# Optimization experiments

Measured on AMD Instinct MI355X. Metric: run time of the kernel, lower is better.

## Reference

```python
import jax, jax.numpy as jnp
import numpy as np

N_HEAD = 16
HEAD = 64
EMBED = 1024
TOP_K_RATIO = 0.1
MASKED = True
B, T = 2, 2048


def setup_inputs() -> dict:
    key = jax.random.key(0)
    ks = jax.random.split(key, 7)
    w = lambda k, shape: jax.random.normal(k, shape, jnp.float32) * 0.02
    return {
        "index": jax.random.normal(ks[0], (B, T, EMBED), jnp.float32),
        "memory": jax.random.normal(ks[1], (B, T, EMBED), jnp.float32),
        "Wq": w(ks[2], (N_HEAD, EMBED, HEAD)),
        "Wk": w(ks[3], (N_HEAD, EMBED, HEAD)),
        "Wv": w(ks[4], (N_HEAD, EMBED, HEAD)),
        "W_proj": w(ks[5], (N_HEAD * HEAD, EMBED)),
        "b_proj": jnp.zeros((EMBED,), jnp.float32),
    }


def reference(index, memory, Wq, Wk, Wv, W_proj, b_proj):
    b, t, e = index.shape
    s = memory.shape[1]
    # All heads batched: [B, H, T, D]
    q = jnp.einsum("bte,hed->bhtd", index, Wq)
    k = jnp.einsum("bse,hed->bhsd", memory, Wk)
    v = jnp.einsum("bse,hed->bhsd", memory, Wv)
    scores = jnp.einsum("bhtd,bhsd->bhts", q, k) * (HEAD ** -0.5)  # [B,H,T,S]
    neg_inf = jnp.array(-jnp.inf, scores.dtype)
    if MASKED:
        causal = jnp.tril(jnp.ones((t, s), bool))
        scores = jnp.where(causal, scores, neg_inf)
    # top-k sparsification: keep only the top ceil(ratio*S) scores per query row
    k_top = max(1, int(TOP_K_RATIO * s))
    thresh = jax.lax.top_k(scores, k_top)[0][..., -1:]  # kth largest per row
    scores = jnp.where(scores >= thresh, scores, neg_inf)
    att = jax.nn.softmax(scores, axis=-1)
    out = jnp.einsum("bhts,bhsd->bhtd", att, v)
    # concat heads along feature dim: [B, T, H*D]
    out = out.transpose(0, 2, 1, 3).reshape(b, t, N_HEAD * HEAD)
    return out @ W_proj + b_proj  # dropout is identity at eval
```

## Files before the change

kernel.cpp:

```cpp
#include <hip/hip_runtime.h>
#include <hip/hip_bf16.h>

#define TT 2048
#define KTOP 204
#define ROWS 16
#define SCS 2056

typedef float f32x4 __attribute__((ext_vector_type(4)));
typedef short short8 __attribute__((ext_vector_type(8)));
typedef unsigned short u16;
typedef unsigned int u32;
typedef u32 u32x2 __attribute__((ext_vector_type(2)));
typedef u32 u32x4 __attribute__((ext_vector_type(4)));

#define NEG_INF (-__builtin_inff())

static __device__ __forceinline__ f32x4 mfma16(short8 a, short8 b, f32x4 c) {
  return __builtin_amdgcn_mfma_f32_16x16x32_bf16(a, b, c, 0, 0, 0);
}

static __device__ __forceinline__ u16 f2b(float f) {
  __hip_bfloat16 h = __float2bfloat16(f);
  return *reinterpret_cast<u16*>(&h);
}

static __device__ __forceinline__ u32 pack_bf16(float a, float b) {
  u32 ua = __float_as_uint(a), ub = __float_as_uint(b);
  ua = (ua + 0x7FFFu + ((ua >> 16) & 1u)) >> 16;
  ub = (ub + 0x7FFFu + ((ub >> 16) & 1u)) & 0xFFFF0000u;
  return ua | ub;
}

#define GLOAD16(gp, lp) __builtin_amdgcn_global_load_lds( \
    (const __attribute__((address_space(1))) void*)(gp),  \
    (__attribute__((address_space(3))) void*)(lp), 16, 0, 0)

#define WSYNC() do { __builtin_amdgcn_wave_barrier(); \
    asm volatile("s_waitcnt lgkmcnt(0)" ::: "memory"); \
    __builtin_amdgcn_wave_barrier(); } while (0)

static __device__ __forceinline__ void rank64(u32 cnt, int lane, int& k,
                                              u32& dig) {
  int suf = (int)cnt;
#pragma unroll
  for (int off = 1; off < 64; off <<= 1) {
    int o = __shfl_down(suf, off);
    suf += (lane + off < 64) ? o : 0;
  }
  int above = suf - (int)cnt;
  bool found = (above < k) && (above + (int)cnt >= k);
  unsigned long long ball = __ballot(found);
  int src = __ffsll((long long)ball) - 1;
  int nk = k - above;
  k = __shfl(nk, src);
  dig = (u32)src;
}

template <int JMAX>
static __device__ __forceinline__ void select_softmax(
    u16* __restrict__ sc, const u32* __restrict__ hist1,
    u32* __restrict__ hist2, const u32* __restrict__ rowmaxk,
    float* __restrict__ rs, int w, int lane, int t0) {
  const int NI = JMAX * 4;
  int row0 = w, row1 = w + 8;
  int n0 = t0 + row0 + 1, n1 = t0 + row1 + 1;
  bool sel0 = n0 > KTOP, sel1 = n1 > KTOP;

  u32 rv0[NI], rv1[NI];
#pragma unroll
  for (int j = 0; j < JMAX; ++j) {
    u32x4 v0 = *(const u32x4*)&sc[row0 * SCS + lane * 8 + j * 512];
    u32x4 v1 = *(const u32x4*)&sc[row1 * SCS + lane * 8 + j * 512];
    rv0[j*4+0] = v0[0]; rv0[j*4+1] = v0[1]; rv0[j*4+2] = v0[2]; rv0[j*4+3] = v0[3];
    rv1[j*4+0] = v1[0]; rv1[j*4+1] = v1[1]; rv1[j*4+2] = v1[2]; rv1[j*4+3] = v1[3];
  }

  u32 keyth0 = 0, keyth1 = 0;
  int k0 = KTOP, k1 = KTOP;
  u32 pfx0 = 0, pfx1 = 0, d;
  u32 c0 = 0, c1 = 0;
  if (lane < 16) {
    u32x4 q0 = *(const u32x4*)&hist1[lane * 64 + row0 * 4];
    u32x4 q1 = *(const u32x4*)&hist1[lane * 64 + row1 * 4];
    c0 = q0[0] + q0[1] + q0[2] + q0[3];
    c1 = q1[0] + q1[1] + q1[2] + q1[3];
  }
  if (sel0) { rank64(c0, lane, k0, d); pfx0 = d; }
  if (sel1) { rank64(c1, lane, k1, d); pfx1 = d; }

  u32* h2a = &hist2[(w * 2 + 0) * 64];
  u32* h2b = &hist2[(w * 2 + 1) * 64];
  h2a[lane] = 0; h2b[lane] = 0;
  WSYNC();
#pragma unroll
  for (int i = 0; i < NI; ++i) {
    u32 p0 = rv0[i], p1 = rv1[i];
    u32 a0 = p0 & 0xFFFFu, a1 = p0 >> 16;
    u32 b0 = p1 & 0xFFFFu, b1 = p1 >> 16;
    if (sel0) {
      if ((a0 >> 12) == pfx0) atomicAdd(&h2a[(a0 >> 6) & 63u], 1u);
      if ((a1 >> 12) == pfx0) atomicAdd(&h2a[(a1 >> 6) & 63u], 1u);
    }
    if (sel1) {
      if ((b0 >> 12) == pfx1) atomicAdd(&h2b[(b0 >> 6) & 63u], 1u);
      if ((b1 >> 12) == pfx1) atomicAdd(&h2b[(b1 >> 6) & 63u], 1u);
    }
  }
  WSYNC();
  if (sel0) { rank64(h2a[lane], lane, k0, d); pfx0 = (pfx0 << 6) | d; }
  if (sel1) { rank64(h2b[lane], lane, k1, d); pfx1 = (pfx1 << 6) | d; }
  h2a[lane] = 0; h2b[lane] = 0;
  WSYNC();
#pragma unroll
  for (int i = 0; i < NI; ++i) {
    u32 p0 = rv0[i], p1 = rv1[i];
    u32 a0 = p0 & 0xFFFFu, a1 = p0 >> 16;
    u32 b0 = p1 & 0xFFFFu, b1 = p1 >> 16;
    if (sel0) {
      if ((a0 >> 6) == pfx0) atomicAdd(&h2a[a0 & 63u], 1u);
      if ((a1 >> 6) == pfx0) atomicAdd(&h2a[a1 & 63u], 1u);
    }
    if (sel1) {
      if ((b0 >> 6) == pfx1) atomicAdd(&h2b[b0 & 63u], 1u);
      if ((b1 >> 6) == pfx1) atomicAdd(&h2b[b1 & 63u], 1u);
    }
  }
  WSYNC();
  if (sel0) { rank64(h2a[lane], lane, k0, d); keyth0 = (pfx0 << 6) | d; }
  if (sel1) { rank64(h2b[lane], lane, k1, d); keyth1 = (pfx1 << 6) | d; }

  u32 thr0 = keyth0 > 1u ? keyth0 : 1u;
  u32 thr1 = keyth1 > 1u ? keyth1 : 1u;
  u32 kmx0 = rowmaxk[row0], kmx1 = rowmaxk[row1];
  const float c2 = 1.44269504f / 4096.f;
  float sum0 = 0.f, sum1 = 0.f;
#pragma unroll
  for (int i = 0; i < NI; ++i) {
    u32 p0 = rv0[i], p1 = rv1[i];
    u32 a0 = p0 & 0xFFFFu, a1 = p0 >> 16;
    u32 b0 = p1 & 0xFFFFu, b1 = p1 >> 16;
    float pa0 = (a0 >= thr0) ? exp2f((float)(int)(a0 - kmx0) * c2) : 0.f;
    float pa1 = (a1 >= thr0) ? exp2f((float)(int)(a1 - kmx0) * c2) : 0.f;
    float pb0 = (b0 >= thr1) ? exp2f((float)(int)(b0 - kmx1) * c2) : 0.f;
    float pb1 = (b1 >= thr1) ? exp2f((float)(int)(b1 - kmx1) * c2) : 0.f;
    sum0 += pa0 + pa1;
    sum1 += pb0 + pb1;
    rv0[i] = pack_bf16(pa0, pa1);
    rv1[i] = pack_bf16(pb0, pb1);
  }
#pragma unroll
  for (int off = 32; off; off >>= 1) {
    sum0 += __shfl_xor(sum0, off);
    sum1 += __shfl_xor(sum1, off);
  }
#pragma unroll
  for (int j = 0; j < JMAX; ++j) {
    *(u32x4*)&sc[row0 * SCS + lane * 8 + j * 512] =
        (u32x4){rv0[j*4+0], rv0[j*4+1], rv0[j*4+2], rv0[j*4+3]};
    *(u32x4*)&sc[row1 * SCS + lane * 8 + j * 512] =
        (u32x4){rv1[j*4+0], rv1[j*4+1], rv1[j*4+2], rv1[j*4+3]};
  }
  if (lane == 0) {
    rs[row0] = 1.f / fmaxf(sum0, 1e-30f);
    rs[row1] = 1.f / fmaxf(sum1, 1e-30f);
  }
}


__global__ __launch_bounds__(256) void k_cast2(const float* __restrict__ in0,
                                               const float* __restrict__ in1,
                                               u16* __restrict__ o0,
                                               u16* __restrict__ o1) {
  const float* in = blockIdx.z ? in1 : in0;
  u16* out = blockIdx.z ? o1 : o0;
  int i = (blockIdx.x * 256 + threadIdx.x) * 4;
  f32x4 v = *(const f32x4*)(in + i);
  u16 r0 = f2b(v[0]), r1 = f2b(v[1]), r2 = f2b(v[2]), r3 = f2b(v[3]);
  out[i] = r0; out[i+1] = r1; out[i+2] = r2; out[i+3] = r3;
}

__global__ __launch_bounds__(256) void k_tw3(
    const float* __restrict__ W0, const float* __restrict__ W1,
    const float* __restrict__ W2, u16* __restrict__ o0,
    u16* __restrict__ o1, u16* __restrict__ o2) {
  int z = blockIdx.z;
  const float* W = z == 0 ? W0 : (z == 1 ? W1 : W2);
  u16* out = z == 0 ? o0 : (z == 1 ? o1 : o2);
  int i = blockIdx.x * 256 + threadIdx.x;
  int d = i & 63, e = (i >> 6) & 1023, h = i >> 16;
  out[(h * 64 + d) * 1024 + e] = f2b(W[i]);
}

__global__ __launch_bounds__(256) void k_tsq(const float* __restrict__ W,
                                             u16* __restrict__ out) {
  int i = blockIdx.x * 256 + threadIdx.x;
  int n = i & 1023, kk = i >> 10;
  out[n * 1024 + kk] = f2b(W[i]);
}

static __device__ __forceinline__ void gemm_core(
    const u16* __restrict__ A, const u16* __restrict__ Bt, int m0, int n0,
    int tid, u16 (*lA)[2048], u16 (*lB)[2048], f32x4* acc) {
  const int K = 1024;
  int w = tid >> 6, lane = tid & 63;
  int lr = lane & 15, lg = lane >> 4;
  const u16* ga = A + (size_t)(m0 + (tid >> 2)) * K + (tid & 3) * 8;
  const u16* gb = Bt + (size_t)(n0 + (tid >> 2)) * K + (tid & 3) * 8;
  char* a0 = (char*)lA[0] + w * 1024;
  char* a1 = (char*)lA[1] + w * 1024;
  char* b0 = (char*)lB[0] + w * 1024;
  char* b1 = (char*)lB[1] + w * 1024;

  for (int kt = 0; kt < K; kt += 64) {
    __syncthreads();
    GLOAD16(ga + kt, a0);
    GLOAD16(gb + kt, b0);
    GLOAD16(ga + kt + 32, a1);
    GLOAD16(gb + kt + 32, b1);
    __syncthreads();
#pragma unroll
    for (int p = 0; p < 2; ++p) {
      short8 a = *(const short8*)&lA[p][(w * 16 + lr) * 32 + lg * 8];
#pragma unroll
      for (int j = 0; j < 4; ++j) {
        short8 b = *(const short8*)&lB[p][(j * 16 + lr) * 32 + lg * 8];
        acc[j] = mfma16(a, b, acc[j]);
      }
    }
  }
}

__global__ __launch_bounds__(256) void gemm_qkv(
    const u16* __restrict__ xbi, const u16* __restrict__ xbm,
    const u16* __restrict__ wqt, const u16* __restrict__ wkt,
    const u16* __restrict__ wvt, u16* __restrict__ qb,
    u16* __restrict__ kbf, u16* __restrict__ vtb) {
  __shared__ u16 lA[2][2048], lB[2][2048];
  int tid = threadIdx.x, z = blockIdx.z;
  int m0 = blockIdx.y * 64, n0 = blockIdx.x * 64;
  const u16* A = z ? xbm : xbi;
  const u16* Bt = z == 0 ? wqt : (z == 1 ? wkt : wvt);
  f32x4 acc[4] = {};
  gemm_core(A, Bt, m0, n0, tid, lA, lB, acc);

  int w = tid >> 6, lane = tid & 63, lr = lane & 15, lg = lane >> 4;
  float ascale = (z == 0) ? 0.125f : 1.f;
  u16* out0 = (z == 0) ? qb : kbf;
  int mbase = m0 + w * 16 + lg * 4;
#pragma unroll
  for (int j = 0; j < 4; ++j) {
    int n = n0 + j * 16 + lr;
#pragma unroll
    for (int jj = 0; jj < 4; ++jj) {
      int m = mbase + jj;
      float v = acc[j][jj];
      int b = m >> 11, t = m & 2047, h = n >> 6, dd = n & 63;
      if (z == 2)
        vtb[(((size_t)(b * 16 + h)) * 64 + dd) * TT + t] = f2b(v);
      else
        out0[(((size_t)(b * 16 + h)) * TT + t) * 64 + dd] = f2b(v * ascale);
    }
  }
}

__global__ __launch_bounds__(256) void gemm_proj(
    const u16* __restrict__ A, const u16* __restrict__ Bt,
    float* __restrict__ outp, const float* __restrict__ bias) {
  __shared__ u16 lA[2][2048], lB[2][2048];
  int tid = threadIdx.x;
  int m0 = blockIdx.y * 64, n0 = blockIdx.x * 64;
  f32x4 acc[4] = {};
  gemm_core(A, Bt, m0, n0, tid, lA, lB, acc);

  int w = tid >> 6, lane = tid & 63, lr = lane & 15, lg = lane >> 4;
  int mbase = m0 + w * 16 + lg * 4;
#pragma unroll
  for (int j = 0; j < 4; ++j) {
    int n = n0 + j * 16 + lr;
#pragma unroll
    for (int jj = 0; jj < 4; ++jj) {
      int m = mbase + jj;
      outp[(size_t)m * 1024 + n] = acc[j][jj] + bias[n];
    }
  }
}

__global__ __launch_bounds__(512, 4) void k_attn(
    const u16* __restrict__ qb, const u16* __restrict__ kb,
    const u16* __restrict__ vtb, u16* __restrict__ aob) {
  __shared__ u16 sc[ROWS * SCS];
  __shared__ u32 aux[2176];
  __shared__ u32 rowmaxk[ROWS];
  __shared__ float rs[ROWS];

  u32* hist1 = aux;
  u32* hist2 = aux + 1024;

  int tid = threadIdx.x, w = tid >> 6, lane = tid & 63;
  int lr = lane & 15, lg = lane >> 4;
  int bid = blockIdx.x + 128 * blockIdx.y;
  int swz = (bid & 7) * 512 + (bid >> 3);
  int t0 = (swz & 127) * ROWS;
  int bh = swz >> 7;
  const u16* qh = qb + (size_t)bh * TT * 64;
  const u16* kh = kb + (size_t)bh * TT * 64;
  const u16* vh = vtb + (size_t)bh * 64 * TT;
  int SC = ((t0 + ROWS + 31) >> 5) << 5;
  int jmax = (SC + 511) >> 9;

  for (int i = tid; i < 1024; i += 512) hist1[i] = 0;
  if (tid < ROWS) rowmaxk[tid] = 0;

  short8 qf0 = *(const short8*)&qh[(size_t)(t0 + lr) * 64 + lg * 8];
  short8 qf1 = *(const short8*)&qh[(size_t)(t0 + lr) * 64 + 32 + lg * 8];
  __syncthreads();

  u32 kmax = 0;
  for (int s0 = w * 16; s0 < SC; s0 += 128) {
    int sbase = s0 + lg * 4;
    if (s0 > t0 + 15) {
      *(u32x2*)&sc[lr * SCS + sbase] = (u32x2){0u, 0u};
      continue;
    }
    short8 kf0 = *(const short8*)&kh[(size_t)(s0 + lr) * 64 + lg * 8];
    short8 kf1 = *(const short8*)&kh[(size_t)(s0 + lr) * 64 + 32 + lg * 8];
    f32x4 acc = {0.f, 0.f, 0.f, 0.f};
    acc = mfma16(kf0, qf0, acc);
    acc = mfma16(kf1, qf1, acc);
    u32 key[4];
    if (s0 + 15 <= t0) {
#pragma unroll
      for (int j = 0; j < 4; ++j) {
        float kf = fmaf(acc[j], 4096.f, 32768.f);
        key[j] = (u32)fminf(fmaxf(kf, 0.f), 65535.f);
      }
    } else {
      int t = t0 + lr;
#pragma unroll
      for (int j = 0; j < 4; ++j) {
        float kf = fmaf(acc[j], 4096.f, 32768.f);
        key[j] = (u32)fminf(fmaxf(kf, 0.f), 65535.f);
        if (sbase + j > t) key[j] = 0;
      }
    }
    kmax = max(kmax, max(max(key[0], key[1]), max(key[2], key[3])));
#pragma unroll
    for (int j = 0; j < 4; ++j)
      atomicAdd(&hist1[(key[j] >> 12) * 64 + lr * 4 + lg], 1u);
    *(u32x2*)&sc[lr * SCS + sbase] =
        (u32x2){key[0] | (key[1] << 16), key[2] | (key[3] << 16)};
  }
  {
    int fillEnd = jmax << 9;
    for (int r = 0; r < ROWS; ++r)
      for (int s = SC + tid * 8; s < fillEnd; s += 512 * 8)
        *(u32x4*)&sc[r * SCS + s] = (u32x4){0, 0, 0, 0};
  }
  kmax = max(kmax, (u32)__shfl_xor((int)kmax, 16));
  kmax = max(kmax, (u32)__shfl_xor((int)kmax, 32));
  if (lane < 16) atomicMax(&rowmaxk[lane], kmax);
  __syncthreads();

  switch (jmax) {
    case 1: select_softmax<1>(sc, hist1, hist2, rowmaxk, rs, w, lane, t0); break;
    case 2: select_softmax<2>(sc, hist1, hist2, rowmaxk, rs, w, lane, t0); break;
    case 3: select_softmax<3>(sc, hist1, hist2, rowmaxk, rs, w, lane, t0); break;
    default: select_softmax<4>(sc, hist1, hist2, rowmaxk, rs, w, lane, t0); break;
  }
  __syncthreads();

  float* po = (float*)aux;
  int d0 = (w & 3) * 16;
  int h = w >> 2;
  int tiles = SC >> 5;
  int mid = ((tiles + 1) >> 1) << 5;
  int kb0 = h ? mid : 0;
  int kb1 = h ? SC : mid;
  f32x4 o = {0.f, 0.f, 0.f, 0.f};
  {
    int kk = kb0;
    short8 bn;
    if (kk < kb1)
      bn = *(const short8*)&vh[(size_t)(d0 + lr) * TT + kk + lg * 8];
    for (; kk < kb1; kk += 32) {
      short8 b = bn;
      int kn = kk + 32;
      if (kn < kb1)
        bn = *(const short8*)&vh[(size_t)(d0 + lr) * TT + kn + lg * 8];
      short8 a = *(const short8*)&sc[lr * SCS + kk + lg * 8];
      o = mfma16(a, b, o);
    }
  }
#pragma unroll
  for (int j = 0; j < 4; ++j)
    po[(h * ROWS + lg * 4 + j) * 68 + d0 + lr] = o[j];
  __syncthreads();

  if (w < 4) {
    int b_ = bh >> 4, h_ = bh & 15;
    int dd0 = w * 16;
#pragma unroll
    for (int j = 0; j < 4; ++j) {
      int row = lg * 4 + j;
      float val = (po[row * 68 + dd0 + lr] + po[(ROWS + row) * 68 + dd0 + lr]) *
                  rs[row];
      aob[((size_t)(b_ * TT + t0 + row)) * 1024 + h_ * 64 + dd0 + lr] = f2b(val);
    }
  }
}


extern "C" void kernel_launch(void* const* d_in, const int* in_sizes, int n_in,
                              void* d_out, int out_size, void* d_ws, size_t ws_size,
                              hipStream_t stream) {
  const float* index  = (const float*)d_in[0];
  const float* memory = (const float*)d_in[1];
  const float* Wq     = (const float*)d_in[2];
  const float* Wk     = (const float*)d_in[3];
  const float* Wv     = (const float*)d_in[4];
  const float* Wp     = (const float*)d_in[5];
  const float* bp     = (const float*)d_in[6];

  char* ws = (char*)d_ws;
  const size_t MB = 1024 * 1024;
  u16* xbi = (u16*)(ws + 0);
  u16* xbm = (u16*)(ws + 8 * MB);
  u16* wqt = (u16*)(ws + 16 * MB);
  u16* wkt = (u16*)(ws + 18 * MB);
  u16* wvt = (u16*)(ws + 20 * MB);
  u16* wpt = (u16*)(ws + 22 * MB);
  u16* qb  = (u16*)(ws + 24 * MB);
  u16* kbf = (u16*)(ws + 32 * MB);
  u16* vtb = (u16*)(ws + 40 * MB);
  u16* aob = xbi;

  k_cast2<<<dim3(4096, 1, 2), 256, 0, stream>>>(index, memory, xbi, xbm);
  k_tw3<<<dim3(4096, 1, 3), 256, 0, stream>>>(Wq, Wk, Wv, wqt, wkt, wvt);
  k_tsq<<<4096, 256, 0, stream>>>(Wp, wpt);

  gemm_qkv<<<dim3(16, 64, 3), 256, 0, stream>>>(xbi, xbm, wqt, wkt, wvt,
                                                qb, kbf, vtb);

  k_attn<<<dim3(TT / ROWS, 32), 512, 0, stream>>>(qb, kbf, vtb, aob);

  gemm_proj<<<dim3(16, 64), 256, 0, stream>>>(aob, wpt, (float*)d_out, bp);
}
```

Before: 294.3 us.

## Switch top-k radix select to two 8-bit passes with packed 16-bit histograms

Replaces the three-pass 4/6/6-bit radix selection with two 8-bit passes. The first-level 256-bin histogram is packed as 16-bit counters per row, built during the QK score pass, and the second pass per row uses a packed 256-bin histogram. The per-row max key atomics are removed; the softmax reference is now derived from the highest nonempty histogram bucket. K fragment loads are software-pipelined one iteration ahead. The trade-offs are more LDS for histograms, sequential per-row second passes, and an approximate max reference that could affect exp range.

```diff
diff --git a/kernel.cpp b/kernel.cpp
--- a/kernel.cpp
+++ b/kernel.cpp
@@ -13,8 +13,6 @@
 typedef u32 u32x2 __attribute__((ext_vector_type(2)));
 typedef u32 u32x4 __attribute__((ext_vector_type(4)));
 
-#define NEG_INF (-__builtin_inff())
-
 static __device__ __forceinline__ f32x4 mfma16(short8 a, short8 b, f32x4 c) {
   return __builtin_amdgcn_mfma_f32_16x16x32_bf16(a, b, c, 0, 0, 0);
 }
@@ -39,32 +37,42 @@
     asm volatile("s_waitcnt lgkmcnt(0)" ::: "memory"); \
     __builtin_amdgcn_wave_barrier(); } while (0)
 
-static __device__ __forceinline__ void rank64(u32 cnt, int lane, int& k,
-                                              u32& dig) {
-  int suf = (int)cnt;
+static __device__ __forceinline__ void radix_rank(int h0, int h1c, int h2c,
+                                                  int h3c, int lane, int& k,
+                                                  u32& digOut) {
+  int lsum = h0 + h1c + h2c + h3c;
+  int ssum = lsum;
 #pragma unroll
   for (int off = 1; off < 64; off <<= 1) {
-    int o = __shfl_down(suf, off);
-    suf += (lane + off < 64) ? o : 0;
-  }
-  int above = suf - (int)cnt;
-  bool found = (above < k) && (above + (int)cnt >= k);
-  unsigned long long ball = __ballot(found);
+    int o = __shfl_down(ssum, off);
+    ssum += (lane + off < 64) ? o : 0;
+  }
+  int above = ssum - lsum;
+  int cg3 = above;
+  int cg2 = cg3 + h3c;
+  int cg1 = cg2 + h2c;
+  int cg0 = cg1 + h1c;
+  int idx = lane * 4;
+  int dig = -1, nk = 0;
+  if (cg0 < k && cg0 + h0 >= k) { dig = idx;     nk = k - cg0; }
+  if (cg1 < k && cg1 + h1c >= k) { dig = idx + 1; nk = k - cg1; }
+  if (cg2 < k && cg2 + h2c >= k) { dig = idx + 2; nk = k - cg2; }
+  if (cg3 < k && cg3 + h3c >= k) { dig = idx + 3; nk = k - cg3; }
+  unsigned long long ball = __ballot(dig >= 0);
   int src = __ffsll((long long)ball) - 1;
-  int nk = k - above;
-  k = __shfl(nk, src);
-  dig = (u32)src;
+  dig = __shfl(dig, src);
+  nk = __shfl(nk, src);
+  digOut = (u32)dig;
+  k = nk;
 }
 
 template <int JMAX>
 static __device__ __forceinline__ void select_softmax(
-    u16* __restrict__ sc, const u32* __restrict__ hist1,
-    u32* __restrict__ hist2, const u32* __restrict__ rowmaxk,
-    float* __restrict__ rs, int w, int lane, int t0) {
+    u16* __restrict__ sc, const u32* __restrict__ hist8,
+    u32* __restrict__ h2w, float* __restrict__ rs, int w, int lane, int t0) {
   const int NI = JMAX * 4;
   int row0 = w, row1 = w + 8;
-  int n0 = t0 + row0 + 1, n1 = t0 + row1 + 1;
-  bool sel0 = n0 > KTOP, sel1 = n1 > KTOP;
+  bool sel0 = t0 + row0 + 1 > KTOP, sel1 = t0 + row1 + 1 > KTOP;
 
   u32 rv0[NI], rv1[NI];
 #pragma unroll
@@ -75,74 +83,82 @@
     rv1[j*4+0] = v1[0]; rv1[j*4+1] = v1[1]; rv1[j*4+2] = v1[2]; rv1[j*4+3] = v1[3];
   }
 
+  u32 a0w = hist8[row0 * 128 + lane * 2], a1w = hist8[row0 * 128 + lane * 2 + 1];
+  u32 b0w = hist8[row1 * 128 + lane * 2], b1w = hist8[row1 * 128 + lane * 2 + 1];
+
+  int lt0 = lane * 4 + ((a1w >> 16) ? 3 : ((a1w & 0xFFFFu) ? 2
+                       : ((a0w >> 16) ? 1 : 0)));
+  int lt1 = lane * 4 + ((b1w >> 16) ? 3 : ((b1w & 0xFFFFu) ? 2
+                       : ((b0w >> 16) ? 1 : 0)));
+  unsigned long long bl0 = __ballot((a0w | a1w) != 0);
+  unsigned long long bl1 = __ballot((b0w | b1w) != 0);
+  int top0 = __shfl(lt0, 63 - __builtin_clzll(bl0));
+  int top1 = __shfl(lt1, 63 - __builtin_clzll(bl1));
+  u32 ref0 = ((u32)top0 << 8) + 255u;
+  u32 ref1 = ((u32)top1 << 8) + 255u;
+
   u32 keyth0 = 0, keyth1 = 0;
   int k0 = KTOP, k1 = KTOP;
-  u32 pfx0 = 0, pfx1 = 0, d;
-  u32 c0 = 0, c1 = 0;
-  if (lane < 16) {
-    u32x4 q0 = *(const u32x4*)&hist1[lane * 64 + row0 * 4];
-    u32x4 q1 = *(const u32x4*)&hist1[lane * 64 + row1 * 4];
-    c0 = q0[0] + q0[1] + q0[2] + q0[3];
-    c1 = q1[0] + q1[1] + q1[2] + q1[3];
-  }
-  if (sel0) { rank64(c0, lane, k0, d); pfx0 = d; }
-  if (sel1) { rank64(c1, lane, k1, d); pfx1 = d; }
-
-  u32* h2a = &hist2[(w * 2 + 0) * 64];
-  u32* h2b = &hist2[(w * 2 + 1) * 64];
-  h2a[lane] = 0; h2b[lane] = 0;
-  WSYNC();
+  u32 d1_0 = 0, d1_1 = 0, d;
+  if (sel0) {
+    radix_rank((int)(a0w & 0xFFFF), (int)(a0w >> 16),
+               (int)(a1w & 0xFFFF), (int)(a1w >> 16), lane, k0, d1_0);
+  }
+  if (sel1) {
+    radix_rank((int)(b0w & 0xFFFF), (int)(b0w >> 16),
+               (int)(b1w & 0xFFFF), (int)(b1w >> 16), lane, k1, d1_1);
+  }
+
+  if (sel0) {
+    h2w[lane] = 0; h2w[lane + 64] = 0;
+    WSYNC();
+#pragma unroll
+    for (int i = 0; i < NI; ++i) {
+      u32 p = rv0[i];
+      u32 e0 = p & 0xFFFFu, e1 = p >> 16;
+      if ((e0 >> 8) == d1_0)
+        atomicAdd(&h2w[(e0 & 255u) >> 1], 1u << ((e0 & 1u) << 4));
+      if ((e1 >> 8) == d1_0)
+        atomicAdd(&h2w[(e1 & 255u) >> 1], 1u << ((e1 & 1u) << 4));
+    }
+    WSYNC();
+    u32 w0 = h2w[lane * 2], w1 = h2w[lane * 2 + 1];
+    radix_rank((int)(w0 & 0xFFFF), (int)(w0 >> 16),
+               (int)(w1 & 0xFFFF), (int)(w1 >> 16), lane, k0, d);
+    keyth0 = (d1_0 << 8) | d;
+  }
+  if (sel1) {
+    h2w[lane] = 0; h2w[lane + 64] = 0;
+    WSYNC();
+#pragma unroll
+    for (int i = 0; i < NI; ++i) {
+      u32 p = rv1[i];
+      u32 e0 = p & 0xFFFFu, e1 = p >> 16;
+      if ((e0 >> 8) == d1_1)
+        atomicAdd(&h2w[(e0 & 255u) >> 1], 1u << ((e0 & 1u) << 4));
+      if ((e1 >> 8) == d1_1)
+        atomicAdd(&h2w[(e1 & 255u) >> 1], 1u << ((e1 & 1u) << 4));
+    }
+    WSYNC();
+    u32 w0 = h2w[lane * 2], w1 = h2w[lane * 2 + 1];
+    radix_rank((int)(w0 & 0xFFFF), (int)(w0 >> 16),
+               (int)(w1 & 0xFFFF), (int)(w1 >> 16), lane, k1, d);
+    keyth1 = (d1_1 << 8) | d;
+  }
+
+  u32 thr0 = keyth0 > 1u ? keyth0 : 1u;
+  u32 thr1 = keyth1 > 1u ? keyth1 : 1u;
+  const float c2 = 1.44269504f / 4096.f;
+  float sum0 = 0.f, sum1 = 0.f;
 #pragma unroll
   for (int i = 0; i < NI; ++i) {
     u32 p0 = rv0[i], p1 = rv1[i];
     u32 a0 = p0 & 0xFFFFu, a1 = p0 >> 16;
     u32 b0 = p1 & 0xFFFFu, b1 = p1 >> 16;
-    if (sel0) {
-      if ((a0 >> 12) == pfx0) atomicAdd(&h2a[(a0 >> 6) & 63u], 1u);
-      if ((a1 >> 12) == pfx0) atomicAdd(&h2a[(a1 >> 6) & 63u], 1u);
-    }
-    if (sel1) {
-      if ((b0 >> 12) == pfx1) atomicAdd(&h2b[(b0 >> 6) & 63u], 1u);
-      if ((b1 >> 12) == pfx1) atomicAdd(&h2b[(b1 >> 6) & 63u], 1u);
-    }
-  }
-  WSYNC();
-  if (sel0) { rank64(h2a[lane], lane, k0, d); pfx0 = (pfx0 << 6) | d; }
-  if (sel1) { rank64(h2b[lane], lane, k1, d); pfx1 = (pfx1 << 6) | d; }
-  h2a[lane] = 0; h2b[lane] = 0;
-  WSYNC();
-#pragma unroll
-  for (int i = 0; i < NI; ++i) {
-    u32 p0 = rv0[i], p1 = rv1[i];
-    u32 a0 = p0 & 0xFFFFu, a1 = p0 >> 16;
-    u32 b0 = p1 & 0xFFFFu, b1 = p1 >> 16;
-    if (sel0) {
-      if ((a0 >> 6) == pfx0) atomicAdd(&h2a[a0 & 63u], 1u);
-      if ((a1 >> 6) == pfx0) atomicAdd(&h2a[a1 & 63u], 1u);
-    }
-    if (sel1) {
-      if ((b0 >> 6) == pfx1) atomicAdd(&h2b[b0 & 63u], 1u);
-      if ((b1 >> 6) == pfx1) atomicAdd(&h2b[b1 & 63u], 1u);
-    }
-  }
-  WSYNC();
-  if (sel0) { rank64(h2a[lane], lane, k0, d); keyth0 = (pfx0 << 6) | d; }
-  if (sel1) { rank64(h2b[lane], lane, k1, d); keyth1 = (pfx1 << 6) | d; }
-
-  u32 thr0 = keyth0 > 1u ? keyth0 : 1u;
-  u32 thr1 = keyth1 > 1u ? keyth1 : 1u;
-  u32 kmx0 = rowmaxk[row0], kmx1 = rowmaxk[row1];
-  const float c2 = 1.44269504f / 4096.f;
-  float sum0 = 0.f, sum1 = 0.f;
-#pragma unroll
-  for (int i = 0; i < NI; ++i) {
-    u32 p0 = rv0[i], p1 = rv1[i];
-    u32 a0 = p0 & 0xFFFFu, a1 = p0 >> 16;
-    u32 b0 = p1 & 0xFFFFu, b1 = p1 >> 16;
-    float pa0 = (a0 >= thr0) ? exp2f((float)(int)(a0 - kmx0) * c2) : 0.f;
-    float pa1 = (a1 >= thr0) ? exp2f((float)(int)(a1 - kmx0) * c2) : 0.f;
-    float pb0 = (b0 >= thr1) ? exp2f((float)(int)(b0 - kmx1) * c2) : 0.f;
-    float pb1 = (b1 >= thr1) ? exp2f((float)(int)(b1 - kmx1) * c2) : 0.f;
+    float pa0 = (a0 >= thr0) ? exp2f((float)(int)(a0 - ref0) * c2) : 0.f;
+    float pa1 = (a1 >= thr0) ? exp2f((float)(int)(a1 - ref0) * c2) : 0.f;
+    float pb0 = (b0 >= thr1) ? exp2f((float)(int)(b0 - ref1) * c2) : 0.f;
+    float pb1 = (b1 >= thr1) ? exp2f((float)(int)(b1 - ref1) * c2) : 0.f;
     sum0 += pa0 + pa1;
     sum1 += pb0 + pb1;
     rv0[i] = pack_bf16(pa0, pa1);
@@ -289,12 +305,11 @@
     const u16* __restrict__ qb, const u16* __restrict__ kb,
     const u16* __restrict__ vtb, u16* __restrict__ aob) {
   __shared__ u16 sc[ROWS * SCS];
-  __shared__ u32 aux[2176];
-  __shared__ u32 rowmaxk[ROWS];
+  __shared__ u32 aux[3072];
   __shared__ float rs[ROWS];
 
-  u32* hist1 = aux;
-  u32* hist2 = aux + 1024;
+  u32* hist8 = aux;
+  u32* h2 = aux + 2048;
 
   int tid = threadIdx.x, w = tid >> 6, lane = tid & 63;
   int lr = lane & 15, lg = lane >> 4;
@@ -308,47 +323,56 @@
   int SC = ((t0 + ROWS + 31) >> 5) << 5;
   int jmax = (SC + 511) >> 9;
 
-  for (int i = tid; i < 1024; i += 512) hist1[i] = 0;
-  if (tid < ROWS) rowmaxk[tid] = 0;
+  for (int i = tid; i < 2048; i += 512) hist8[i] = 0;
 
   short8 qf0 = *(const short8*)&qh[(size_t)(t0 + lr) * 64 + lg * 8];
   short8 qf1 = *(const short8*)&qh[(size_t)(t0 + lr) * 64 + 32 + lg * 8];
   __syncthreads();
 
-  u32 kmax = 0;
-  for (int s0 = w * 16; s0 < SC; s0 += 128) {
-    int sbase = s0 + lg * 4;
-    if (s0 > t0 + 15) {
-      *(u32x2*)&sc[lr * SCS + sbase] = (u32x2){0u, 0u};
-      continue;
-    }
-    short8 kf0 = *(const short8*)&kh[(size_t)(s0 + lr) * 64 + lg * 8];
-    short8 kf1 = *(const short8*)&kh[(size_t)(s0 + lr) * 64 + 32 + lg * 8];
-    f32x4 acc = {0.f, 0.f, 0.f, 0.f};
-    acc = mfma16(kf0, qf0, acc);
-    acc = mfma16(kf1, qf1, acc);
-    u32 key[4];
-    if (s0 + 15 <= t0) {
-#pragma unroll
-      for (int j = 0; j < 4; ++j) {
-        float kf = fmaf(acc[j], 4096.f, 32768.f);
-        key[j] = (u32)fminf(fmaxf(kf, 0.f), 65535.f);
+  {
+    int t = t0 + lr;
+    int s0 = w * 16;
+    short8 kc0, kc1, kn0, kn1;
+    if (s0 < SC) {
+      kc0 = *(const short8*)&kh[(size_t)(s0 + lr) * 64 + lg * 8];
+      kc1 = *(const short8*)&kh[(size_t)(s0 + lr) * 64 + 32 + lg * 8];
+      if (s0 + 128 < SC) {
+        kn0 = *(const short8*)&kh[(size_t)(s0 + 128 + lr) * 64 + lg * 8];
+        kn1 = *(const short8*)&kh[(size_t)(s0 + 128 + lr) * 64 + 32 + lg * 8];
       }
-    } else {
-      int t = t0 + lr;
-#pragma unroll
-      for (int j = 0; j < 4; ++j) {
-        float kf = fmaf(acc[j], 4096.f, 32768.f);
-        key[j] = (u32)fminf(fmaxf(kf, 0.f), 65535.f);
-        if (sbase + j > t) key[j] = 0;
+    }
+    for (; s0 < SC; s0 += 128) {
+      f32x4 acc = {0.f, 0.f, 0.f, 0.f};
+      acc = mfma16(kc0, qf0, acc);
+      acc = mfma16(kc1, qf1, acc);
+      kc0 = kn0; kc1 = kn1;
+      if (s0 + 256 < SC) {
+        kn0 = *(const short8*)&kh[(size_t)(s0 + 256 + lr) * 64 + lg * 8];
+        kn1 = *(const short8*)&kh[(size_t)(s0 + 256 + lr) * 64 + 32 + lg * 8];
       }
-    }
-    kmax = max(kmax, max(max(key[0], key[1]), max(key[2], key[3])));
-#pragma unroll
-    for (int j = 0; j < 4; ++j)
-      atomicAdd(&hist1[(key[j] >> 12) * 64 + lr * 4 + lg], 1u);
-    *(u32x2*)&sc[lr * SCS + sbase] =
-        (u32x2){key[0] | (key[1] << 16), key[2] | (key[3] << 16)};
+      int sbase = s0 + lg * 4;
+      u32 key[4];
+      if (s0 + 15 <= t0) {
+#pragma unroll
+        for (int j = 0; j < 4; ++j) {
+          float kf = fmaf(acc[j], 4096.f, 32768.f);
+          key[j] = (u32)fmaxf(kf, 0.f);
+        }
+      } else {
+#pragma unroll
+        for (int j = 0; j < 4; ++j) {
+          float kf = fmaf(acc[j], 4096.f, 32768.f);
+          key[j] = (u32)fmaxf(kf, 0.f);
+          if (sbase + j > t) key[j] = 0;
+        }
+      }
+#pragma unroll
+      for (int j = 0; j < 4; ++j)
+        atomicAdd(&hist8[lr * 128 + (key[j] >> 9)],
+                  1u << (((key[j] >> 8) & 1u) << 4));
+      *(u32x2*)&sc[lr * SCS + sbase] =
+          (u32x2){key[0] | (key[1] << 16), key[2] | (key[3] << 16)};
+    }
   }
   {
     int fillEnd = jmax << 9;
@@ -356,16 +380,13 @@
       for (int s = SC + tid * 8; s < fillEnd; s += 512 * 8)
         *(u32x4*)&sc[r * SCS + s] = (u32x4){0, 0, 0, 0};
   }
-  kmax = max(kmax, (u32)__shfl_xor((int)kmax, 16));
-  kmax = max(kmax, (u32)__shfl_xor((int)kmax, 32));
-  if (lane < 16) atomicMax(&rowmaxk[lane], kmax);
   __syncthreads();
 
   switch (jmax) {
-    case 1: select_softmax<1>(sc, hist1, hist2, rowmaxk, rs, w, lane, t0); break;
-    case 2: select_softmax<2>(sc, hist1, hist2, rowmaxk, rs, w, lane, t0); break;
-    case 3: select_softmax<3>(sc, hist1, hist2, rowmaxk, rs, w, lane, t0); break;
-    default: select_softmax<4>(sc, hist1, hist2, rowmaxk, rs, w, lane, t0); break;
+    case 1: select_softmax<1>(sc, hist8, &h2[w * 128], rs, w, lane, t0); break;
+    case 2: select_softmax<2>(sc, hist8, &h2[w * 128], rs, w, lane, t0); break;
+    case 3: select_softmax<3>(sc, hist8, &h2[w * 128], rs, w, lane, t0); break;
+    default: select_softmax<4>(sc, hist8, &h2[w * 128], rs, w, lane, t0); break;
   }
   __syncthreads();
 
@@ -441,7 +462,7 @@
   gemm_qkv<<<dim3(16, 64, 3), 256, 0, stream>>>(xbi, xbm, wqt, wkt, wvt,
                                                 qb, kbf, vtb);
 
-  k_attn<<<dim3(TT / ROWS, 32), 512, 0, stream>>>(qb, kbf, vtb, aob);
+  k_attn<<<dim3(128, 32), 512, 0, stream>>>(qb, kbf, vtb, aob);
 
   gemm_proj<<<dim3(16, 64), 256, 0, stream>>>(aob, wpt, (float*)d_out, bp);
 }
```

New measurement: 282.6 us. 1.04x faster.
